# Optimization experiments

Hardware: AMD Instinct MI355X
Metric: run time of the kernel (lower is better)

The kernel has to match this reference:

```python
import jax, jax.numpy as jnp
import numpy as np

L, B, CIN, H, W = 32, 4, 3, 16, 16
D, HEADS, DK, DEPTH = 64, 4, 16, 2
EPS = 1e-5
BN_INV = float(1.0 / np.sqrt(1.0 + EPS))  # eval-mode BatchNorm with default stats/affine


def conv2d(x, w, b=None, pad=1, groups=1):
    y = jax.lax.conv_general_dilated(
        x, w, window_strides=(1, 1), padding=[(pad, pad), (pad, pad)],
        dimension_numbers=('NCHW', 'OIHW', 'NCHW'), feature_group_count=groups)
    if b is not None:
        y = y + b[None, :, None, None]
    return y


def layer_norm(x, w, b):
    # LayerNorm over last 3 dims [D,H,W] of (L,B,D,H,W)
    mu = jnp.mean(x, axis=(-3, -2, -1), keepdims=True)
    var = jnp.var(x, axis=(-3, -2, -1), keepdims=True)
    return (x - mu) * jax.lax.rsqrt(var + EPS) * w + b


def pos_table():
    pos = jnp.arange(L, dtype=jnp.float32)
    exp = (2.0 * (jnp.arange(D) // 2).astype(jnp.float32)) / D
    angle = pos[:, None] / jnp.power(10000.0, exp)[None, :]  # (L, D)
    # source applies sin to even POSITIONS and cos to odd POSITIONS (table[0::2]=sin)
    tab = jnp.where((jnp.arange(L) % 2 == 0)[:, None], jnp.sin(angle), jnp.cos(angle))
    return tab[:, None, :, None, None]  # (L,1,D,1,1) broadcast over B,H,W


def reference(x, gw1, gb1, gw2, gb2, gw3, gb3, gw4, gb4,
              conv1_w, conv1_b, conv2_w, conv2_b, wq, wk, wv, w0,
              ln1_w, ln1_b, ln2_w, ln2_b, ff_w1, ff_b1, ff_w2, ff_b2):
    lrelu = lambda v: jax.nn.leaky_relu(v, 0.01)
    h = x.reshape(L * B, CIN, H, W)
    for w_, b_ in ((gw1, gb1), (gw2, gb2), (gw3, gb3), (gw4, gb4)):
        h = lrelu(conv2d(h, w_, b_) * BN_INV)
    xlb = h.reshape(L, B, D, H, W) + pos_table()

    for i in range(DEPTH):
        # ---- multi-head conv attention (dec=True) ----
        y = layer_norm(xlb, ln1_w[i], ln1_b[i])
        xa = jnp.transpose(y, (1, 2, 3, 4, 0))  # (B,D,H,W,L)
        # conv1 is a 1x1 conv == pointwise linear over channels, per head
        qkv = jnp.einsum('bchwl,noc->bnohwl', xa, conv1_w[i]) \
            + conv1_b[i][None, :, :, None, None, None]  # (B,HEADS,3D,H,W,L)
        q, k, v = jnp.split(qkv, 3, axis=2)  # each (B,HEADS,D,H,W,L)
        q = jnp.einsum('bnchwl,nck->bnkhwl', q, wq[i])  # (B,HEADS,DK,H,W,L)
        k = jnp.einsum('bnchwl,nck->bnkhwl', k, wk[i])
        v = jnp.einsum('bnchwl,nck->bnkhwl', v, wv[i])

        def head_conv(t):
            # 5x5 conv per head (no bias): conv2(Q_i + K_j) = conv_w(Q)_i + conv_w(K)_j + bias
            z = jnp.transpose(t, (0, 5, 1, 2, 3, 4)).reshape(B * L, HEADS * DK, H, W)
            z = conv2d(z, conv2_w[i].reshape(HEADS * DK, DK, 5, 5), None, pad=2, groups=HEADS)
            return jnp.transpose(z.reshape(B, L, HEADS, DK, H, W), (0, 2, 3, 4, 5, 1))

        cq = head_conv(q)
        ck = head_conv(k)
        logits = cq[..., :, None] + ck[..., None, :] \
            + conv2_b[i][None, :, :, None, None, None, None]  # (B,HEADS,DK,H,W,Lq,Lk)
        a = jax.nn.softmax(logits, axis=-1)
        vout = jnp.einsum('bnkhwij,bnkhwj->bnkhwi', a, v)   # (B,HEADS,DK,H,W,L)
        vcat = vout.reshape(B, D, H, W, L)                  # concat heads on channel dim
        attn = jnp.einsum('bchwl,co->bohwl', vcat, w0[i])
        xlb = xlb + jnp.transpose(attn, (4, 0, 1, 2, 3))

        # ---- feed-forward over the TIME dimension (Linear on L) ----
        y = layer_norm(xlb, ln2_w[i], ln2_b[i])
        xp = jnp.transpose(y, (1, 2, 3, 4, 0))  # (B,D,H,W,L)
        h1 = lrelu(jnp.einsum('bchwl,ml->bchwm', xp, ff_w1[i]) + ff_b1[i])
        ff = jnp.einsum('bchwm,lm->bchwl', h1, ff_w2[i]) + ff_b2[i]
        xlb = xlb + jnp.transpose(ff, (4, 0, 1, 2, 3))
    return xlb


def setup_inputs() -> dict:
    key = jax.random.key(0)
    specs = {
        'x': (L, B, CIN, H, W),
        'gw1': (4, 3, 3, 3), 'gb1': (4,), 'gw2': (6, 4, 3, 3), 'gb2': (6,),
        'gw3': (8, 6, 3, 3), 'gb3': (8,), 'gw4': (64, 8, 3, 3), 'gb4': (64,),
        'conv1_w': (DEPTH, HEADS, 3 * D, D), 'conv1_b': (DEPTH, HEADS, 3 * D),
        'conv2_w': (DEPTH, HEADS, DK, DK, 5, 5), 'conv2_b': (DEPTH, HEADS, DK),
        'wq': (DEPTH, HEADS, D, DK), 'wk': (DEPTH, HEADS, D, DK), 'wv': (DEPTH, HEADS, D, DK),
        'w0': (DEPTH, D, D),
        'ln1_w': (DEPTH, D, H, W), 'ln1_b': (DEPTH, D, H, W),
        'ln2_w': (DEPTH, D, H, W), 'ln2_b': (DEPTH, D, H, W),
        'ff_w1': (DEPTH, 4 * L, L), 'ff_b1': (DEPTH, 4 * L),
        'ff_w2': (DEPTH, L, 4 * L), 'ff_b2': (DEPTH, L),
    }
    out = {}
    for idx, (name, shape) in enumerate(specs.items()):
        g = jax.random.normal(jax.random.fold_in(key, idx), shape, dtype=jnp.float32)
        if name == 'x':
            out[name] = g
        elif name in ('ln1_w', 'ln2_w'):
            out[name] = 1.0 + 0.05 * g
        else:
            out[name] = 0.05 * g
    return out
```

## Files before the change

kernel.cpp:

```cpp
#include <hip/hip_runtime.h>
#include <math.h>

#define LL 32
#define BB 4
#define DD 64
#define NH 4
#define DKK 16
#define BN_INV 0.9999950000374997f

__device__ __forceinline__ float lrelu(float v){ return v > 0.f ? v : 0.01f*v; }

__device__ __forceinline__ float wave_sum(float v){
  #pragma unroll
  for(int off=1; off<64; off<<=1) v += __shfl_xor(v, off, 64);
  return v;
}

__global__ __launch_bounds__(256) void k_prep(
    const float* __restrict__ c1w, const float* __restrict__ c1b,
    const float* __restrict__ wk,  const float* __restrict__ wv,
    const float* __restrict__ w2,  const float* __restrict__ gw4,
    const float* __restrict__ ffw2,
    const float* __restrict__ x,
    const float* __restrict__ gw1, const float* __restrict__ gb1,
    const float* __restrict__ gw2, const float* __restrict__ gb2,
    const float* __restrict__ gw3, const float* __restrict__ gb3,
    float* __restrict__ A, float* __restrict__ bf, float* __restrict__ pos,
    float* __restrict__ wT, float* __restrict__ wT3, float* __restrict__ w2T,
    float* __restrict__ out8, float* __restrict__ stats){
  __shared__ float sh[4212];
  int blk = blockIdx.x, t = threadIdx.x;
  if(blk < 64){
    int tid = blk*256 + t;
    int k = tid & 15, d = (tid>>4)&63, n=(tid>>10)&3, tt=(tid>>12)&1, i=tid>>13;
    const float* wsel = (tt ? wv : wk) + (i*NH+n)*64*16;
    const float* cw   = c1w + ((i*NH+n)*192 + (tt+1)*64)*64;
    float acc = 0.f;
    for(int c=0;c<64;++c) acc += cw[c*64+d]*wsel[c*16+k];
    A[tid] = acc;
    if(d==0){
      const float* cb = c1b + (i*NH+n)*192 + (tt+1)*64;
      float ba=0.f;
      for(int c=0;c<64;++c) ba += cb[c]*wsel[c*16+k];
      bf[((i*2+tt)*4+n)*16+k] = ba;
    }
  } else if(blk < 72){
    int tid = (blk-64)*256 + t;
    int d = tid & 63, l = tid >> 6;
    float ex = (float)(d>>1) / 32.0f;
    float angle = (float)l * powf(10000.0f, -ex);
    pos[tid] = (l & 1) ? cosf(angle) : sinf(angle);
  } else if(blk < 272){
    int tid = (blk-72)*256 + t;
    int k = tid & 15; int rest = tid >> 4;
    int tap = rest % 25; int rest2 = rest / 25;
    int c = rest2 & 15; int dn = rest2 >> 4;
    wT[tid] = w2[((dn*16 + k)*16 + c)*25 + tap];
  } else if(blk < 290){
    int tid = (blk-272)*256 + t;
    int co = tid & 63, ct = tid >> 6;
    wT3[ct*64 + co] = gw4[co*72 + ct];
  } else if(blk < 322){
    int tid = (blk-290)*256 + t;
    int l = tid & 31; int m = (tid>>5)&127; int dep = tid>>12;
    w2T[tid] = ffw2[dep*4096 + l*128 + m];
  } else if(blk < 450){
    float* T0 = sh; float* T1 = sh + 972; float* T2 = sh + 2268;
    int f = blk - 322;
    int h = t>>4, w = t&15;
    for(int j=t;j<4212;j+=256) sh[j]=0.f;
    __syncthreads();
    for(int ci=0;ci<3;++ci) T0[ci*324 + (h+1)*18 + (w+1)] = x[f*768 + ci*256 + t];
    __syncthreads();
    for(int co=0;co<4;++co){
      float acc = gb1[co];
      for(int ci=0;ci<3;++ci){
        const float* tb = T0 + ci*324 + h*18 + w;
        const float* wb = gw1 + co*27 + ci*9;
        #pragma unroll
        for(int dy=0;dy<3;++dy)
          #pragma unroll
          for(int dx=0;dx<3;++dx) acc += tb[dy*18+dx]*wb[dy*3+dx];
      }
      T1[co*324 + (h+1)*18 + (w+1)] = lrelu(acc*BN_INV);
    }
    __syncthreads();
    for(int co=0;co<6;++co){
      float acc = gb2[co];
      for(int ci=0;ci<4;++ci){
        const float* tb = T1 + ci*324 + h*18 + w;
        const float* wb = gw2 + co*36 + ci*9;
        #pragma unroll
        for(int dy=0;dy<3;++dy)
          #pragma unroll
          for(int dx=0;dx<3;++dx) acc += tb[dy*18+dx]*wb[dy*3+dx];
      }
      T2[co*324 + (h+1)*18 + (w+1)] = lrelu(acc*BN_INV);
    }
    __syncthreads();
    for(int co=0;co<8;++co){
      float acc = gb3[co];
      for(int ci=0;ci<6;++ci){
        const float* tb = T2 + ci*324 + h*18 + w;
        const float* wb = gw3 + co*54 + ci*9;
        #pragma unroll
        for(int dy=0;dy<3;++dy)
          #pragma unroll
          for(int dx=0;dx<3;++dx) acc += tb[dy*18+dx]*wb[dy*3+dx];
      }
      out8[f*2048 + co*256 + t] = lrelu(acc*BN_INV);
    }
  } else {
    stats[t] = 0.f;
  }
}

__global__ __launch_bounds__(256) void k_conv3_l4(const float* __restrict__ in8,
    const float* __restrict__ wT3, const float* __restrict__ gb4,
    const float* __restrict__ pos, float* __restrict__ out,
    float* __restrict__ nst){
  __shared__ float tile[8*324];
  __shared__ float wsl[1152];
  int blk = blockIdx.x; int g = blk & 3; int f = blk >> 2;
  int t = threadIdx.x; int h = t>>4, w = t&15;
  for(int j=t;j<2592;j+=256) tile[j]=0.f;
  for(int j=t;j<1152;j+=256){
    int ct = j>>4, c16 = j&15;
    wsl[j] = wT3[ct*64 + g*16 + c16];
  }
  __syncthreads();
  for(int ci=0;ci<8;++ci) tile[ci*324 + (h+1)*18 + (w+1)] = in8[f*2048 + ci*256 + t];
  __syncthreads();
  float acc[16];
  #pragma unroll
  for(int q=0;q<16;++q) acc[q] = gb4[g*16+q];
  for(int ci=0;ci<8;++ci){
    const float* tb = tile + ci*324 + h*18 + w;
    #pragma unroll
    for(int dy=0;dy<3;++dy){
      #pragma unroll
      for(int dx=0;dx<3;++dx){
        float v = tb[dy*18+dx];
        const float* wp = wsl + (ci*9+dy*3+dx)*16;
        float4 wa = *(const float4*)(wp);
        float4 wb = *(const float4*)(wp+4);
        float4 wc = *(const float4*)(wp+8);
        float4 wd = *(const float4*)(wp+12);
        acc[0]+=v*wa.x; acc[1]+=v*wa.y; acc[2]+=v*wa.z; acc[3]+=v*wa.w;
        acc[4]+=v*wb.x; acc[5]+=v*wb.y; acc[6]+=v*wb.z; acc[7]+=v*wb.w;
        acc[8]+=v*wc.x; acc[9]+=v*wc.y; acc[10]+=v*wc.z; acc[11]+=v*wc.w;
        acc[12]+=v*wd.x; acc[13]+=v*wd.y; acc[14]+=v*wd.z; acc[15]+=v*wd.w;
      }
    }
  }
  int l = f >> 2;
  float s = 0.f, s2 = 0.f;
  #pragma unroll
  for(int q=0;q<16;++q){
    float r = lrelu(acc[q]*BN_INV) + pos[l*64 + g*16 + q];
    out[f*16384 + (g*16+q)*256 + t] = r;
    s += r; s2 += r*r;
  }
  float ws_ = wave_sum(s), ws2 = wave_sum(s2);
  if((t & 63) == 0){
    atomicAdd(&nst[f*2],   ws_);
    atomicAdd(&nst[f*2+1], ws2);
  }
}

__global__ __launch_bounds__(1024) void k_stats(const float* __restrict__ x,
                                                float* __restrict__ stats){
  int g = blockIdx.x, t = threadIdx.x;
  const float4* xb = (const float4*)(x + g*16384);
  float s=0.f, s2=0.f;
  #pragma unroll
  for(int j=0;j<4;++j){
    float4 v = xb[t + j*1024];
    s  += v.x + v.y + v.z + v.w;
    s2 += v.x*v.x + v.y*v.y + v.z*v.z + v.w*v.w;
  }
  __shared__ float ls[1024], ls2[1024];
  ls[t]=s; ls2[t]=s2; __syncthreads();
  for(int off=512;off>0;off>>=1){
    if(t<off){ ls[t]+=ls[t+off]; ls2[t]+=ls2[t+off]; }
    __syncthreads();
  }
  if(t==0){
    stats[g*2]   = ls[0];
    stats[g*2+1] = ls2[0];
  }
}

__global__ __launch_bounds__(256, 1) void k_kvc5(const float* __restrict__ x,
     const float* __restrict__ lnw, const float* __restrict__ lnb,
     const float* __restrict__ st,
     const float* __restrict__ A, const float* __restrict__ bf,
     const float* __restrict__ wT,
     float* __restrict__ V, float* __restrict__ CK, int dep){
  __shared__ float tile[16*480];
  int blk = blockIdx.x;
  int n = blk & 3; int lb = blk >> 2;
  int t = threadIdx.x; int h = t>>4, w = t&15;
  for(int j=t;j<7680;j+=256) tile[j]=0.f;
  float mu = st[lb*2]*(1.0f/16384.f);
  float ri = rsqrtf(st[lb*2+1]*(1.0f/16384.f) - mu*mu + 1e-5f);
  const float* xb  = x   + lb*16384 + t;
  const float* wbp = lnw + t;
  const float* bbp = lnb + t;
  const float* akb = A + ((dep*2+0)*4+n)*1024;
  const float* avb = A + ((dep*2+1)*4+n)*1024;
  float kacc[16], vacc[16];
  #pragma unroll
  for(int q=0;q<16;++q){
    kacc[q] = bf[((dep*2+0)*4+n)*16+q];
    vacc[q] = bf[((dep*2+1)*4+n)*16+q];
  }
  #pragma unroll 4
  for(int d=0;d<64;++d){
    float yv = (xb[d*256]-mu)*ri*wbp[d*256] + bbp[d*256];
    const float* ak = akb + d*16;
    const float* av = avb + d*16;
    #pragma unroll
    for(int q=0;q<16;++q){ kacc[q] += yv*ak[q]; vacc[q] += yv*av[q]; }
  }
  int l = lb >> 2, b = lb & 3;
  int fh = (b*32+l)*4+n;
  __syncthreads();
  #pragma unroll
  for(int q=0;q<16;++q){
    V[fh*4096 + q*256 + t] = vacc[q];
    tile[q*480 + (h+2)*24 + (w+2)] = kacc[q];
  }
  __syncthreads();
  const float* wb = wT + (dep*4+n)*6400;
  float acc[16];
  #pragma unroll
  for(int q=0;q<16;++q) acc[q] = 0.f;
  for(int c=0;c<16;++c){
    const float* tb = tile + c*480 + h*24 + w;
    const float* wc = wb + c*400;
    #pragma unroll
    for(int dy=0;dy<5;++dy){
      #pragma unroll
      for(int dx=0;dx<5;++dx){
        float v = tb[dy*24+dx];
        const float* wp = wc + (dy*5+dx)*16;
        float4 wa = *(const float4*)(wp);
        float4 wbv = *(const float4*)(wp+4);
        float4 wcv = *(const float4*)(wp+8);
        float4 wdv = *(const float4*)(wp+12);
        acc[0]+=v*wa.x;  acc[1]+=v*wa.y;  acc[2]+=v*wa.z;  acc[3]+=v*wa.w;
        acc[4]+=v*wbv.x; acc[5]+=v*wbv.y; acc[6]+=v*wbv.z; acc[7]+=v*wbv.w;
        acc[8]+=v*wcv.x; acc[9]+=v*wcv.y; acc[10]+=v*wcv.z; acc[11]+=v*wcv.w;
        acc[12]+=v*wdv.x; acc[13]+=v*wdv.y; acc[14]+=v*wdv.z; acc[15]+=v*wdv.w;
      }
    }
  }
  float* ob = CK + fh*4096;
  #pragma unroll
  for(int q=0;q<16;++q) ob[q*256+t] = acc[q];
}

__global__ void k_soft(const float* __restrict__ CK, const float* __restrict__ V,
                       float* __restrict__ vout){
  int idx = blockIdx.x*256 + threadIdx.x;
  int p = idx&255; int k=(idx>>8)&15; int n=(idx>>12)&3; int b=idx>>14;
  int base = (b*128 + n)*4096 + k*256 + p;
  float e[32]; float m = -1e30f;
  for(int l=0;l<32;++l){ float v = CK[base + l*16384]; e[l]=v; m = fmaxf(m,v); }
  float s = 0.f;
  for(int l=0;l<32;++l){ e[l] = expf(e[l]-m); s += e[l]; }
  float inv = 1.f/s, acc = 0.f;
  for(int l=0;l<32;++l) acc += e[l]*V[base + l*16384];
  vout[((b*4+n)*16+k)*256+p] = acc*inv;
}

__global__ void k_w0res(const float* __restrict__ vout, const float* __restrict__ w0,
                        float* __restrict__ xlb, int dep){
  int idx = blockIdx.x*256 + threadIdx.x;
  int p = idx&255; int o=(idx>>8)&63; int b=idx>>14;
  const float* vb = vout + b*64*256 + p;
  const float* wb = w0 + dep*4096 + o;
  float acc = 0.f;
  for(int c=0;c<64;++c) acc += vb[c*256]*wb[c*64];
  for(int l=0;l<32;++l) xlb[((l*4+b)*64+o)*256 + p] += acc;
}

__global__ __launch_bounds__(256) void k_ff(float* __restrict__ xlb,
                     const float* __restrict__ lnw, const float* __restrict__ lnb,
                     const float* __restrict__ stats,
                     const float* __restrict__ w1, const float* __restrict__ b1,
                     const float* __restrict__ w2T, const float* __restrict__ b2,
                     int dep){
  __shared__ float pfa[4*2048];
  int t = threadIdx.x;
  int lane = t & 63;
  int w = __builtin_amdgcn_readfirstlane(t >> 6);
  int blk = blockIdx.x;
  int elem = blk*64 + lane;
  int b = blk >> 8;
  int e = elem & 16383;
  float lw  = lnw[e];
  float lbv = lnb[e];
  float yv[32];
  #pragma unroll
  for(int l=0;l<32;++l){
    float mu = stats[(l*4+b)*2]*(1.0f/16384.f);
    float ri = rsqrtf(stats[(l*4+b)*2+1]*(1.0f/16384.f) - mu*mu + 1e-5f);
    float xv = xlb[elem + l*65536];
    yv[l] = (xv-mu)*ri*lw + lbv;
  }
  float fa[32];
  if(w==0){
    #pragma unroll
    for(int l=0;l<32;++l) fa[l] = b2[dep*32+l];
  } else {
    #pragma unroll
    for(int l=0;l<32;++l) fa[l] = 0.f;
  }
  const float* w1b  = w1  + dep*4096 + w*1024;
  const float* w2Tb = w2T + dep*4096 + w*1024;
  const float* b1b  = b1  + dep*128  + w*32;
  #pragma unroll 4
  for(int mm=0;mm<32;++mm){
    float s0=0.f,s1=0.f,s2=0.f,s3=0.f;
    #pragma unroll
    for(int l=0;l<32;l+=4){
      s0 += yv[l+0]*w1b[mm*32+l+0];
      s1 += yv[l+1]*w1b[mm*32+l+1];
      s2 += yv[l+2]*w1b[mm*32+l+2];
      s3 += yv[l+3]*w1b[mm*32+l+3];
    }
    float s = lrelu(((s0+s1)+(s2+s3)) + b1b[mm]);
    #pragma unroll
    for(int l=0;l<32;++l) fa[l] += s*w2Tb[mm*32+l];
  }
  #pragma unroll
  for(int l=0;l<32;++l) pfa[w*2048 + l*64 + lane] = fa[l];
  __syncthreads();
  #pragma unroll
  for(int j=0;j<8;++j){
    int pi = t + j*256;
    float sum = pfa[pi] + pfa[pi+2048] + pfa[pi+4096] + pfa[pi+6144];
    int l = pi >> 6, ln2 = pi & 63;
    int ix = blk*64 + ln2 + l*65536;
    xlb[ix] = xlb[ix] + sum;
  }
}

extern "C" void kernel_launch(void* const* d_in, const int* in_sizes, int n_in,
                              void* d_out, int out_size, void* d_ws, size_t ws_size,
                              hipStream_t stream) {
  const float* x       = (const float*)d_in[0];
  const float* gw1     = (const float*)d_in[1];
  const float* gb1     = (const float*)d_in[2];
  const float* gw2     = (const float*)d_in[3];
  const float* gb2     = (const float*)d_in[4];
  const float* gw3     = (const float*)d_in[5];
  const float* gb3     = (const float*)d_in[6];
  const float* gw4     = (const float*)d_in[7];
  const float* gb4     = (const float*)d_in[8];
  const float* conv1_w = (const float*)d_in[9];
  const float* conv1_b = (const float*)d_in[10];
  const float* conv2_w = (const float*)d_in[11];
  const float* wk      = (const float*)d_in[14];
  const float* wv      = (const float*)d_in[15];
  const float* w0      = (const float*)d_in[16];
  const float* ln1_w   = (const float*)d_in[17];
  const float* ln1_b   = (const float*)d_in[18];
  const float* ln2_w   = (const float*)d_in[19];
  const float* ln2_b   = (const float*)d_in[20];
  const float* ff_w1   = (const float*)d_in[21];
  const float* ff_b1   = (const float*)d_in[22];
  const float* ff_w2   = (const float*)d_in[23];
  const float* ff_b2   = (const float*)d_in[24];

  float* out = (float*)d_out;
  float* ws  = (float*)d_ws;
  float* CK    = ws;
  float* V     = ws + 2097152;
  float* vout  = ws + 4194304;
  float* A     = ws + 4259840;
  float* bf    = ws + 4276224;
  float* pos   = ws + 4276480;
  float* wT    = ws + 4278528;
  float* wT3   = ws + 4329728;
  float* w2T   = ws + 4334336;
  float* stats = ws + 4342528;

  k_prep<<<451, 256, 0, stream>>>(conv1_w, conv1_b, wk, wv, conv2_w, gw4, ff_w2,
                                  x, gw1, gb1, gw2, gb2, gw3, gb3,
                                  A, bf, pos, wT, wT3, w2T, CK, stats);
  k_conv3_l4<<<512, 256, 0, stream>>>(CK, wT3, gb4, pos, out, stats);

  for(int dep=0; dep<2; ++dep){
    if(dep==1) k_stats<<<128, 1024, 0, stream>>>(out, stats);
    k_kvc5 <<<512,  256, 0, stream>>>(out, ln1_w + dep*16384, ln1_b + dep*16384,
                                      stats, A, bf, wT, V, CK, dep);
    k_soft <<<256,  256, 0, stream>>>(CK, V, vout);
    k_w0res<<<256,  256, 0, stream>>>(vout, w0, out, dep);
    k_stats<<<128, 1024, 0, stream>>>(out, stats);
    k_ff   <<<1024, 256, 0, stream>>>(out, ln2_w + dep*16384, ln2_b + dep*16384,
                                      stats, ff_w1, ff_b1, w2T, ff_b2, dep);
  }
}
```

Baseline: 330.0 us.

## Split k_kvc5 output channels across four thread groups per block

k_kvc5 now runs 1024 threads per block. Each group of 256 threads handles 4 of the 16 K/V output channels, where previously one thread computed all 16. This cuts per-thread register use and raises occupancy and parallelism for the LN+projection and 5x5 conv stages. In exchange, the layernorm input loads and the shared tile reads in the conv are repeated by each of the four groups.

Result: slower. 481.7 us (+46.0%).

```diff
diff --git a/kernel.cpp b/kernel.cpp
--- a/kernel.cpp
+++ b/kernel.cpp
@@ -191,7 +191,7 @@
   }
 }
 
-__global__ __launch_bounds__(256, 1) void k_kvc5(const float* __restrict__ x,
+__global__ __launch_bounds__(1024) void k_kvc5(const float* __restrict__ x,
      const float* __restrict__ lnw, const float* __restrict__ lnb,
      const float* __restrict__ st,
      const float* __restrict__ A, const float* __restrict__ bf,
@@ -200,42 +200,43 @@
   __shared__ float tile[16*480];
   int blk = blockIdx.x;
   int n = blk & 3; int lb = blk >> 2;
-  int t = threadIdx.x; int h = t>>4, w = t&15;
-  for(int j=t;j<7680;j+=256) tile[j]=0.f;
+  int t = threadIdx.x;
+  int kq = t >> 8;
+  int p  = t & 255;
+  int h = p>>4, w = p&15;
+  for(int j=t;j<7680;j+=1024) tile[j]=0.f;
   float mu = st[lb*2]*(1.0f/16384.f);
   float ri = rsqrtf(st[lb*2+1]*(1.0f/16384.f) - mu*mu + 1e-5f);
-  const float* xb  = x   + lb*16384 + t;
-  const float* wbp = lnw + t;
-  const float* bbp = lnb + t;
-  const float* akb = A + ((dep*2+0)*4+n)*1024;
-  const float* avb = A + ((dep*2+1)*4+n)*1024;
-  float kacc[16], vacc[16];
-  #pragma unroll
-  for(int q=0;q<16;++q){
-    kacc[q] = bf[((dep*2+0)*4+n)*16+q];
-    vacc[q] = bf[((dep*2+1)*4+n)*16+q];
-  }
-  #pragma unroll 4
+  const float* xb  = x   + lb*16384 + p;
+  const float* wbp = lnw + p;
+  const float* bbp = lnb + p;
+  const float* akb = A + ((dep*2+0)*4+n)*1024 + kq*4;
+  const float* avb = A + ((dep*2+1)*4+n)*1024 + kq*4;
+  float kacc[4], vacc[4];
+  #pragma unroll
+  for(int q=0;q<4;++q){
+    kacc[q] = bf[((dep*2+0)*4+n)*16 + kq*4 + q];
+    vacc[q] = bf[((dep*2+1)*4+n)*16 + kq*4 + q];
+  }
   for(int d=0;d<64;++d){
     float yv = (xb[d*256]-mu)*ri*wbp[d*256] + bbp[d*256];
-    const float* ak = akb + d*16;
-    const float* av = avb + d*16;
-    #pragma unroll
-    for(int q=0;q<16;++q){ kacc[q] += yv*ak[q]; vacc[q] += yv*av[q]; }
+    float4 ak4 = *(const float4*)(akb + d*16);
+    float4 av4 = *(const float4*)(avb + d*16);
+    kacc[0]+=yv*ak4.x; kacc[1]+=yv*ak4.y; kacc[2]+=yv*ak4.z; kacc[3]+=yv*ak4.w;
+    vacc[0]+=yv*av4.x; vacc[1]+=yv*av4.y; vacc[2]+=yv*av4.z; vacc[3]+=yv*av4.w;
   }
   int l = lb >> 2, b = lb & 3;
   int fh = (b*32+l)*4+n;
   __syncthreads();
   #pragma unroll
-  for(int q=0;q<16;++q){
-    V[fh*4096 + q*256 + t] = vacc[q];
-    tile[q*480 + (h+2)*24 + (w+2)] = kacc[q];
+  for(int q=0;q<4;++q){
+    int k = kq*4 + q;
+    V[fh*4096 + k*256 + p] = vacc[q];
+    tile[k*480 + (h+2)*24 + (w+2)] = kacc[q];
   }
   __syncthreads();
-  const float* wb = wT + (dep*4+n)*6400;
-  float acc[16];
-  #pragma unroll
-  for(int q=0;q<16;++q) acc[q] = 0.f;
+  const float* wb = wT + (dep*4+n)*6400 + kq*4;
+  float acc[4] = {0.f,0.f,0.f,0.f};
   for(int c=0;c<16;++c){
     const float* tb = tile + c*480 + h*24 + w;
     const float* wc = wb + c*400;
@@ -244,21 +245,14 @@
       #pragma unroll
       for(int dx=0;dx<5;++dx){
         float v = tb[dy*24+dx];
-        const float* wp = wc + (dy*5+dx)*16;
-        float4 wa = *(const float4*)(wp);
-        float4 wbv = *(const float4*)(wp+4);
-        float4 wcv = *(const float4*)(wp+8);
-        float4 wdv = *(const float4*)(wp+12);
-        acc[0]+=v*wa.x;  acc[1]+=v*wa.y;  acc[2]+=v*wa.z;  acc[3]+=v*wa.w;
-        acc[4]+=v*wbv.x; acc[5]+=v*wbv.y; acc[6]+=v*wbv.z; acc[7]+=v*wbv.w;
-        acc[8]+=v*wcv.x; acc[9]+=v*wcv.y; acc[10]+=v*wcv.z; acc[11]+=v*wcv.w;
-        acc[12]+=v*wdv.x; acc[13]+=v*wdv.y; acc[14]+=v*wdv.z; acc[15]+=v*wdv.w;
+        float4 w4 = *(const float4*)(wc + (dy*5+dx)*16);
+        acc[0]+=v*w4.x; acc[1]+=v*w4.y; acc[2]+=v*w4.z; acc[3]+=v*w4.w;
       }
     }
   }
-  float* ob = CK + fh*4096;
-  #pragma unroll
-  for(int q=0;q<16;++q) ob[q*256+t] = acc[q];
+  float* ob = CK + fh*4096 + kq*4*256;
+  #pragma unroll
+  for(int q=0;q<4;++q) ob[q*256 + p] = acc[q];
 }
 
 __global__ void k_soft(const float* __restrict__ CK, const float* __restrict__ V,
@@ -395,7 +389,7 @@
 
   for(int dep=0; dep<2; ++dep){
     if(dep==1) k_stats<<<128, 1024, 0, stream>>>(out, stats);
-    k_kvc5 <<<512,  256, 0, stream>>>(out, ln1_w + dep*16384, ln1_b + dep*16384,
+    k_kvc5 <<<512, 1024, 0, stream>>>(out, ln1_w + dep*16384, ln1_b + dep*16384,
                                       stats, A, bf, wT, V, CK, dep);
     k_soft <<<256,  256, 0, stream>>>(CK, V, vout);
     k_w0res<<<256,  256, 0, stream>>>(vout, w0, out, dep);
```
